# Optimization experiments

Measured on AMD Instinct MI355X. Metric: run time of the kernel, lower is better.

## Reference

```python
import jax, jax.numpy as jnp
import numpy as np

OUT_F = 2048
IN_F = 2048
NNZ = 209715  # int(0.05 * OUT_F * IN_F)
ALPHA = 1.0


def setup_inputs() -> dict:
    key = jax.random.key(0)
    k1, k2, k3, k4, k5, k6 = jax.random.split(key, 6)
    x = jax.random.normal(k1, (4, 4096, IN_F), dtype=jnp.float32)
    # two int4 nibbles (offset-by-8 codes in [0,15]) packed per byte
    base_packed = jax.random.randint(k2, (OUT_F, IN_F // 2), 0, 256, dtype=jnp.int32)
    # per-row scale = row_max/7, strictly positive
    scales = jax.random.uniform(k3, (OUT_F,), dtype=jnp.float32, minval=1e-3, maxval=0.1)
    # sparse residual in COO form (values are small corrections)
    ortho_vals = jax.random.normal(k4, (NNZ,), dtype=jnp.float32) * 0.01
    ortho_rows = jax.random.randint(k5, (NNZ,), 0, OUT_F, dtype=jnp.int32)
    ortho_cols = jax.random.randint(k6, (NNZ,), 0, IN_F, dtype=jnp.int32)
    return {"x": x, "base_packed": base_packed, "scales": scales,
            "ortho_vals": ortho_vals, "ortho_rows": ortho_rows, "ortho_cols": ortho_cols}


def _dequant_base(base_packed, scales):
    # unpack: low nibble -> even input cols, high nibble -> odd input cols
    low = base_packed & 0xF          # [out, in/2]
    high = (base_packed >> 4) & 0xF  # [out, in/2]
    w_offset = jnp.stack([low, high], axis=-1).reshape(OUT_F, IN_F)
    return (w_offset.astype(jnp.float32) - 8.0) * scales[:, None]  # [out, in]


def reference(x, base_packed, scales, ortho_vals, ortho_rows, ortho_cols):
    w_base = _dequant_base(base_packed, scales)
    # scatter sparse residual into dense weight (same size as weight itself)
    w_ortho = jnp.zeros((OUT_F, IN_F), dtype=jnp.float32).at[ortho_rows, ortho_cols].add(ortho_vals)
    W = w_base + ALPHA * w_ortho  # [out, in]
    x_flat = x.reshape(-1, IN_F)  # [tokens, in]
    out = jnp.einsum('ti,oi->to', x_flat, W)
    return out.reshape(x.shape[:-1] + (OUT_F,))
```

## Files before the change

kernel.cpp:

```cpp
#include <hip/hip_runtime.h>
#include <hip/hip_bf16.h>

#define OUT_F 2048
#define IN_F  2048

typedef __attribute__((ext_vector_type(8))) short bfx8;
typedef __attribute__((ext_vector_type(4))) short s16x4;
typedef __attribute__((ext_vector_type(4))) float fx4;

__device__ __forceinline__ unsigned short f2bf(float f) {
  unsigned int u = __float_as_uint(f);
  u += 0x7FFFu + ((u >> 16) & 1u);
  return (unsigned short)(u >> 16);
}

__device__ __forceinline__ void async_copy16(const void* gsrc, void* ldst) {
  __builtin_amdgcn_global_load_lds(
      (const __attribute__((address_space(1))) unsigned int*)gsrc,
      (__attribute__((address_space(3))) unsigned int*)ldst,
      16, 0, 0);
}


__global__ __launch_bounds__(256) void k_dequant(const int* __restrict__ packed,
                                                 const float* __restrict__ scales,
                                                 float* __restrict__ Wf) {
  int i = blockIdx.x * 256 + threadIdx.x;
  int row = i >> 10;
  int v = packed[i];
  float s = scales[row];
  float2 w;
  w.x = (float)((v & 0xF) - 8) * s;
  w.y = (float)(((v >> 4) & 0xF) - 8) * s;
  reinterpret_cast<float2*>(Wf)[i] = w;
}

__global__ __launch_bounds__(256) void k_scatter(const float* __restrict__ vals,
                                                 const int* __restrict__ rows,
                                                 const int* __restrict__ cols,
                                                 float* __restrict__ Wf, int nnz) {
  int i = blockIdx.x * 256 + threadIdx.x;
  if (i < nnz)
    atomicAdd(Wf + (size_t)rows[i] * IN_F + cols[i], vals[i]);
}

__global__ __launch_bounds__(256) void k_f32_to_bf16x8(const float* __restrict__ in,
                                                       short* __restrict__ outp) {
  long long i = (long long)blockIdx.x * 256 + threadIdx.x;
  const float4* v = reinterpret_cast<const float4*>(in) + 2 * i;
  float4 a = v[0], b = v[1];
  bfx8 r;
  r[0] = (short)f2bf(a.x); r[1] = (short)f2bf(a.y);
  r[2] = (short)f2bf(a.z); r[3] = (short)f2bf(a.w);
  r[4] = (short)f2bf(b.x); r[5] = (short)f2bf(b.y);
  r[6] = (short)f2bf(b.z); r[7] = (short)f2bf(b.w);
  reinterpret_cast<bfx8*>(outp)[i] = r;
}


__global__ __launch_bounds__(256) void k_gemm_bt(const short* __restrict__ A,
                                                 const short* __restrict__ B,
                                                 float* __restrict__ C,
                                                 int M, int N, int K) {
  __shared__ __align__(16) short Asm[128 * 32];
  __shared__ __align__(16) short Bsm[128 * 32];

  const int tid  = threadIdx.x;
  const int lane = tid & 63;
  const int wave = tid >> 6;
  const int wr = wave >> 1, wc = wave & 1;
  const int l15 = lane & 15, l16 = lane >> 4;

  int nwg = gridDim.x, bid = blockIdx.x;
  int swz = ((nwg & 7) == 0) ? ((bid & 7) * (nwg >> 3) + (bid >> 3)) : bid;
  int nbn = N / 128;
  int bm = swz / nbn, bn = swz % nbn;

  fx4 acc[4][4] = {};

  const short* Ablk = A + (size_t)bm * 128 * K;
  const short* Bblk = B + (size_t)bn * 128 * K;

  for (int k0 = 0; k0 < K; k0 += 32) {
#pragma unroll
    for (int i = 0; i < 2; ++i) {
      int c = i * 256 + tid;
      int r = c >> 2, kc = (c & 3) * 8;
      const short* ga = Ablk + (size_t)r * K + k0 + kc;
      const short* gb = Bblk + (size_t)r * K + k0 + kc;
      short* la = Asm + i * 2048 + wave * 512;
      short* lb = Bsm + i * 2048 + wave * 512;
      async_copy16(ga, la);
      async_copy16(gb, lb);
    }
    __syncthreads();

    bfx8 a[4], b[4];
#pragma unroll
    for (int mi = 0; mi < 4; ++mi)
      a[mi] = *reinterpret_cast<const bfx8*>(Asm + (wr * 64 + mi * 16 + l15) * 32 + l16 * 8);
#pragma unroll
    for (int ni = 0; ni < 4; ++ni)
      b[ni] = *reinterpret_cast<const bfx8*>(Bsm + (wc * 64 + ni * 16 + l15) * 32 + l16 * 8);
#pragma unroll
    for (int mi = 0; mi < 4; ++mi)
#pragma unroll
      for (int ni = 0; ni < 4; ++ni)
        acc[mi][ni] = __builtin_amdgcn_mfma_f32_16x16x32_bf16(a[mi], b[ni], acc[mi][ni], 0, 0, 0);
    __syncthreads();
  }

  float* Cblk = C + (size_t)(bm * 128 + wr * 64) * N + bn * 128 + wc * 64;
#pragma unroll
  for (int mi = 0; mi < 4; ++mi)
#pragma unroll
    for (int ni = 0; ni < 4; ++ni)
#pragma unroll
      for (int r = 0; r < 4; ++r)
        Cblk[(size_t)(mi * 16 + l16 * 4 + r) * N + ni * 16 + l15] = acc[mi][ni][r];
}

__global__ __launch_bounds__(256) void k_gemm_bt_cvtA(const float* __restrict__ A,
                                                      const short* __restrict__ B,
                                                      float* __restrict__ C,
                                                      int M, int N, int K) {
  __shared__ __align__(16) short Asm[128 * 32];
  __shared__ __align__(16) short Bsm[128 * 32];

  const int tid  = threadIdx.x;
  const int lane = tid & 63;
  const int wave = tid >> 6;
  const int wr = wave >> 1, wc = wave & 1;
  const int l15 = lane & 15, l16 = lane >> 4;

  int nwg = gridDim.x, bid = blockIdx.x;
  int swz = ((nwg & 7) == 0) ? ((bid & 7) * (nwg >> 3) + (bid >> 3)) : bid;
  int nbn = N / 128;
  int bm = swz / nbn, bn = swz % nbn;

  fx4 acc[4][4] = {};

  const float* Ablk = A + (size_t)bm * 128 * K;
  const short* Bblk = B + (size_t)bn * 128 * K;

  for (int k0 = 0; k0 < K; k0 += 32) {
#pragma unroll
    for (int i = 0; i < 2; ++i) {
      int c = i * 256 + tid;
      int r = c >> 2, kc = (c & 3) * 8;
      const short* gb = Bblk + (size_t)r * K + k0 + kc;
      short* lb = Bsm + i * 2048 + wave * 512;
      async_copy16(gb, lb);
    }
#pragma unroll
    for (int i = 0; i < 4; ++i) {
      int c = i * 256 + tid;
      int r = c >> 3, kc = (c & 7) * 4;
      float4 v = *reinterpret_cast<const float4*>(Ablk + (size_t)r * K + k0 + kc);
      s16x4 p;
      p[0] = (short)f2bf(v.x); p[1] = (short)f2bf(v.y);
      p[2] = (short)f2bf(v.z); p[3] = (short)f2bf(v.w);
      *reinterpret_cast<s16x4*>(Asm + r * 32 + kc) = p;
    }
    __syncthreads();

    bfx8 a[4], b[4];
#pragma unroll
    for (int mi = 0; mi < 4; ++mi)
      a[mi] = *reinterpret_cast<const bfx8*>(Asm + (wr * 64 + mi * 16 + l15) * 32 + l16 * 8);
#pragma unroll
    for (int ni = 0; ni < 4; ++ni)
      b[ni] = *reinterpret_cast<const bfx8*>(Bsm + (wc * 64 + ni * 16 + l15) * 32 + l16 * 8);
#pragma unroll
    for (int mi = 0; mi < 4; ++mi)
#pragma unroll
      for (int ni = 0; ni < 4; ++ni)
        acc[mi][ni] = __builtin_amdgcn_mfma_f32_16x16x32_bf16(a[mi], b[ni], acc[mi][ni], 0, 0, 0);
    __syncthreads();
  }

  float* Cblk = C + (size_t)(bm * 128 + wr * 64) * N + bn * 128 + wc * 64;
#pragma unroll
  for (int mi = 0; mi < 4; ++mi)
#pragma unroll
    for (int ni = 0; ni < 4; ++ni)
#pragma unroll
      for (int r = 0; r < 4; ++r)
        Cblk[(size_t)(mi * 16 + l16 * 4 + r) * N + ni * 16 + l15] = acc[mi][ni][r];
}

extern "C" void kernel_launch(void* const* d_in, const int* in_sizes, int n_in,
                              void* d_out, int out_size, void* d_ws, size_t ws_size,
                              hipStream_t stream) {
  const float* x      = (const float*)d_in[0];
  const int*   packed = (const int*)d_in[1];
  const float* scales = (const float*)d_in[2];
  const float* ovals  = (const float*)d_in[3];
  const int*   orows  = (const int*)d_in[4];
  const int*   ocols  = (const int*)d_in[5];
  float* out = (float*)d_out;

  const int tokens = in_sizes[0] / IN_F;
  const int nnz    = in_sizes[3];

  const size_t xb_bytes = (size_t)tokens * IN_F * sizeof(short);
  const size_t wf_bytes = (size_t)OUT_F * IN_F * sizeof(float);
  const size_t wb_bytes = (size_t)OUT_F * IN_F * sizeof(short);

  char* ws = (char*)d_ws;
  const int grid = (tokens / 128) * (OUT_F / 128);

  if (ws_size >= xb_bytes + wf_bytes + wb_bytes) {
    short* xb = (short*)ws;
    float* Wf = (float*)(ws + xb_bytes);
    short* Wb = (short*)(ws + xb_bytes + wf_bytes);

    k_dequant<<<OUT_F * IN_F / 2 / 256, 256, 0, stream>>>(packed, scales, Wf);
    k_scatter<<<(nnz + 255) / 256, 256, 0, stream>>>(ovals, orows, ocols, Wf, nnz);
    k_f32_to_bf16x8<<<OUT_F * IN_F / 8 / 256, 256, 0, stream>>>(Wf, Wb);
    k_f32_to_bf16x8<<<(int)((size_t)tokens * IN_F / 8 / 256), 256, 0, stream>>>(x, xb);
    k_gemm_bt<<<grid, 256, 0, stream>>>(xb, Wb, out, tokens, OUT_F, IN_F);
  } else {
    float* Wf = (float*)ws;
    short* Wb = (short*)(ws + wf_bytes);

    k_dequant<<<OUT_F * IN_F / 2 / 256, 256, 0, stream>>>(packed, scales, Wf);
    k_scatter<<<(nnz + 255) / 256, 256, 0, stream>>>(ovals, orows, ocols, Wf, nnz);
    k_f32_to_bf16x8<<<OUT_F * IN_F / 8 / 256, 256, 0, stream>>>(Wf, Wb);
    k_gemm_bt_cvtA<<<grid, 256, 0, stream>>>(x, Wb, out, tokens, OUT_F, IN_F);
  }
}
```

Baseline: 448.7 us.

## Replace GEMM with 256x256-tile double-buffered swizzled-LDS bf16 MFMA kernel

Replaces the 128x128, K=32 GEMM with a 512-thread kernel that computes 256x256 output tiles using K=64 steps. LDS is double-buffered so the next tile's async global->LDS copies overlap the current tile's MFMAs, and an XOR swizzle on LDS rows avoids bank conflicts. It also raises wave priority around the MFMA block. The fallback path for small workspaces is dropped, so the kernel now assumes the workspace is large enough for the bf16 copy of x.

```diff
diff --git a/kernel.cpp b/kernel.cpp
--- a/kernel.cpp
+++ b/kernel.cpp
@@ -5,7 +5,6 @@
 #define IN_F  2048
 
 typedef __attribute__((ext_vector_type(8))) short bfx8;
-typedef __attribute__((ext_vector_type(4))) short s16x4;
 typedef __attribute__((ext_vector_type(4))) float fx4;
 
 __device__ __forceinline__ unsigned short f2bf(float f) {
@@ -58,135 +57,108 @@
 }
 
 
-__global__ __launch_bounds__(256) void k_gemm_bt(const short* __restrict__ A,
-                                                 const short* __restrict__ B,
-                                                 float* __restrict__ C,
-                                                 int M, int N, int K) {
-  __shared__ __align__(16) short Asm[128 * 32];
-  __shared__ __align__(16) short Bsm[128 * 32];
+__global__ __launch_bounds__(512, 2) void k_gemm256(const short* __restrict__ A,
+                                                    const short* __restrict__ B,
+                                                    float* __restrict__ C,
+                                                    int M, int N, int K) {
+  extern __shared__ short smem[];
+  short* As = smem;
+  short* Bs = smem + 2 * 256 * 64;
 
-  const int tid  = threadIdx.x;
-  const int lane = tid & 63;
-  const int wave = tid >> 6;
-  const int wr = wave >> 1, wc = wave & 1;
-  const int l15 = lane & 15, l16 = lane >> 4;
+  const int tid = threadIdx.x;
+  const int l   = tid & 63;
+  const int w   = tid >> 6;
+  const int wr  = w >> 2;
+  const int wc  = w & 3;
+  const int l15 = l & 15, l16 = l >> 4;
 
   int nwg = gridDim.x, bid = blockIdx.x;
   int swz = ((nwg & 7) == 0) ? ((bid & 7) * (nwg >> 3) + (bid >> 3)) : bid;
-  int nbn = N / 128;
+  int nbn = N >> 8;
   int bm = swz / nbn, bn = swz % nbn;
 
-  fx4 acc[4][4] = {};
+  const short* Ablk = A + (size_t)bm * 256 * K;
+  const short* Bblk = B + (size_t)bn * 256 * K;
 
-  const short* Ablk = A + (size_t)bm * 128 * K;
-  const short* Bblk = B + (size_t)bn * 128 * K;
+  const int srow   = l >> 3;
+  const int srcoff = (((l & 7) ^ (l >> 3)) << 3);
 
-  for (int k0 = 0; k0 < K; k0 += 32) {
+  fx4 acc[8][4] = {};
+  const int NT = K >> 6;
+
 #pragma unroll
-    for (int i = 0; i < 2; ++i) {
-      int c = i * 256 + tid;
-      int r = c >> 2, kc = (c & 3) * 8;
-      const short* ga = Ablk + (size_t)r * K + k0 + kc;
-      const short* gb = Bblk + (size_t)r * K + k0 + kc;
-      short* la = Asm + i * 2048 + wave * 512;
-      short* lb = Bsm + i * 2048 + wave * 512;
-      async_copy16(ga, la);
-      async_copy16(gb, lb);
+  for (int h = 0; h < 2; ++h)
+#pragma unroll
+    for (int j = 0; j < 2; ++j) {
+      int row = h * 128 + w * 16 + j * 8;
+      async_copy16(Ablk + (size_t)(row + srow) * K + srcoff, As + row * 64);
+      async_copy16(Bblk + (size_t)(row + srow) * K + srcoff, Bs + row * 64);
     }
-    __syncthreads();
+  asm volatile("s_waitcnt vmcnt(0)" ::: "memory");
+  __builtin_amdgcn_s_barrier();
 
-    bfx8 a[4], b[4];
+  for (int kt = 0; kt < NT; ++kt) {
+    const int c = kt & 1;
+    const short* Ac = As + c * 256 * 64;
+    const short* Bc = Bs + c * 256 * 64;
+
+    __builtin_amdgcn_s_barrier();
+    __builtin_amdgcn_sched_barrier(0);
+
+    if (kt + 1 < NT) {
+      const int k0 = (kt + 1) << 6;
+      short* An = As + (c ^ 1) * 256 * 64;
+      short* Bn = Bs + (c ^ 1) * 256 * 64;
 #pragma unroll
-    for (int mi = 0; mi < 4; ++mi)
-      a[mi] = *reinterpret_cast<const bfx8*>(Asm + (wr * 64 + mi * 16 + l15) * 32 + l16 * 8);
+      for (int h = 0; h < 2; ++h)
 #pragma unroll
-    for (int ni = 0; ni < 4; ++ni)
-      b[ni] = *reinterpret_cast<const bfx8*>(Bsm + (wc * 64 + ni * 16 + l15) * 32 + l16 * 8);
+        for (int j = 0; j < 2; ++j) {
+          int row = h * 128 + w * 16 + j * 8;
+          async_copy16(Ablk + (size_t)(row + srow) * K + k0 + srcoff, An + row * 64);
+          async_copy16(Bblk + (size_t)(row + srow) * K + k0 + srcoff, Bn + row * 64);
+        }
+      asm volatile("s_waitcnt vmcnt(8)" ::: "memory");
+    } else {
+      asm volatile("s_waitcnt vmcnt(0)" ::: "memory");
+    }
+    __builtin_amdgcn_s_barrier();
+    __builtin_amdgcn_sched_barrier(0);
+
+    bfx8 bf[2][4];
 #pragma unroll
-    for (int mi = 0; mi < 4; ++mi)
+    for (int ks = 0; ks < 2; ++ks)
+#pragma unroll
+      for (int ni = 0; ni < 4; ++ni) {
+        int r = wc * 64 + ni * 16 + l15;
+        bf[ks][ni] = *reinterpret_cast<const bfx8*>(
+            Bc + r * 64 + (((ks * 4 + l16) ^ (l15 & 7)) << 3));
+      }
+    __builtin_amdgcn_s_setprio(1);
+#pragma unroll
+    for (int mi = 0; mi < 8; ++mi) {
+      int r = wr * 128 + mi * 16 + l15;
+      bfx8 a0 = *reinterpret_cast<const bfx8*>(
+          Ac + r * 64 + ((l16 ^ (l15 & 7)) << 3));
+      bfx8 a1 = *reinterpret_cast<const bfx8*>(
+          Ac + r * 64 + (((4 + l16) ^ (l15 & 7)) << 3));
 #pragma unroll
       for (int ni = 0; ni < 4; ++ni)
-        acc[mi][ni] = __builtin_amdgcn_mfma_f32_16x16x32_bf16(a[mi], b[ni], acc[mi][ni], 0, 0, 0);
-    __syncthreads();
+        acc[mi][ni] = __builtin_amdgcn_mfma_f32_16x16x32_bf16(a0, bf[0][ni], acc[mi][ni], 0, 0, 0);
+#pragma unroll
+      for (int ni = 0; ni < 4; ++ni)
+        acc[mi][ni] = __builtin_amdgcn_mfma_f32_16x16x32_bf16(a1, bf[1][ni], acc[mi][ni], 0, 0, 0);
+    }
+    __builtin_amdgcn_s_setprio(0);
   }
 
-  float* Cblk = C + (size_t)(bm * 128 + wr * 64) * N + bn * 128 + wc * 64;
+  float* Cb = C + (size_t)(bm * 256 + wr * 128) * N + bn * 256 + wc * 64;
 #pragma unroll
-  for (int mi = 0; mi < 4; ++mi)
+  for (int mi = 0; mi < 8; ++mi)
 #pragma unroll
     for (int ni = 0; ni < 4; ++ni)
 #pragma unroll
       for (int r = 0; r < 4; ++r)
-        Cblk[(size_t)(mi * 16 + l16 * 4 + r) * N + ni * 16 + l15] = acc[mi][ni][r];
-}
-
-__global__ __launch_bounds__(256) void k_gemm_bt_cvtA(const float* __restrict__ A,
-                                                      const short* __restrict__ B,
-                                                      float* __restrict__ C,
-                                                      int M, int N, int K) {
-  __shared__ __align__(16) short Asm[128 * 32];
-  __shared__ __align__(16) short Bsm[128 * 32];
-
-  const int tid  = threadIdx.x;
-  const int lane = tid & 63;
-  const int wave = tid >> 6;
-  const int wr = wave >> 1, wc = wave & 1;
-  const int l15 = lane & 15, l16 = lane >> 4;
-
-  int nwg = gridDim.x, bid = blockIdx.x;
-  int swz = ((nwg & 7) == 0) ? ((bid & 7) * (nwg >> 3) + (bid >> 3)) : bid;
-  int nbn = N / 128;
-  int bm = swz / nbn, bn = swz % nbn;
-
-  fx4 acc[4][4] = {};
-
-  const float* Ablk = A + (size_t)bm * 128 * K;
-  const short* Bblk = B + (size_t)bn * 128 * K;
-
-  for (int k0 = 0; k0 < K; k0 += 32) {
-#pragma unroll
-    for (int i = 0; i < 2; ++i) {
-      int c = i * 256 + tid;
-      int r = c >> 2, kc = (c & 3) * 8;
-      const short* gb = Bblk + (size_t)r * K + k0 + kc;
-      short* lb = Bsm + i * 2048 + wave * 512;
-      async_copy16(gb, lb);
-    }
-#pragma unroll
-    for (int i = 0; i < 4; ++i) {
-      int c = i * 256 + tid;
-      int r = c >> 3, kc = (c & 7) * 4;
-      float4 v = *reinterpret_cast<const float4*>(Ablk + (size_t)r * K + k0 + kc);
-      s16x4 p;
-      p[0] = (short)f2bf(v.x); p[1] = (short)f2bf(v.y);
-      p[2] = (short)f2bf(v.z); p[3] = (short)f2bf(v.w);
-      *reinterpret_cast<s16x4*>(Asm + r * 32 + kc) = p;
-    }
-    __syncthreads();
-
-    bfx8 a[4], b[4];
-#pragma unroll
-    for (int mi = 0; mi < 4; ++mi)
-      a[mi] = *reinterpret_cast<const bfx8*>(Asm + (wr * 64 + mi * 16 + l15) * 32 + l16 * 8);
-#pragma unroll
-    for (int ni = 0; ni < 4; ++ni)
-      b[ni] = *reinterpret_cast<const bfx8*>(Bsm + (wc * 64 + ni * 16 + l15) * 32 + l16 * 8);
-#pragma unroll
-    for (int mi = 0; mi < 4; ++mi)
-#pragma unroll
-      for (int ni = 0; ni < 4; ++ni)
-        acc[mi][ni] = __builtin_amdgcn_mfma_f32_16x16x32_bf16(a[mi], b[ni], acc[mi][ni], 0, 0, 0);
-    __syncthreads();
-  }
-
-  float* Cblk = C + (size_t)(bm * 128 + wr * 64) * N + bn * 128 + wc * 64;
-#pragma unroll
-  for (int mi = 0; mi < 4; ++mi)
-#pragma unroll
-    for (int ni = 0; ni < 4; ++ni)
-#pragma unroll
-      for (int r = 0; r < 4; ++r)
-        Cblk[(size_t)(mi * 16 + l16 * 4 + r) * N + ni * 16 + l15] = acc[mi][ni][r];
+        Cb[(size_t)(mi * 16 + l16 * 4 + r) * N + ni * 16 + l15] = acc[mi][ni][r];
 }
 
 extern "C" void kernel_launch(void* const* d_in, const int* in_sizes, int n_in,
@@ -205,28 +177,22 @@
 
   const size_t xb_bytes = (size_t)tokens * IN_F * sizeof(short);
   const size_t wf_bytes = (size_t)OUT_F * IN_F * sizeof(float);
-  const size_t wb_bytes = (size_t)OUT_F * IN_F * sizeof(short);
 
   char* ws = (char*)d_ws;
-  const int grid = (tokens / 128) * (OUT_F / 128);
+  short* xb = (short*)ws;
+  float* Wf = (float*)(ws + xb_bytes);
+  short* Wb = (short*)(ws + xb_bytes + wf_bytes);
 
-  if (ws_size >= xb_bytes + wf_bytes + wb_bytes) {
-    short* xb = (short*)ws;
-    float* Wf = (float*)(ws + xb_bytes);
-    short* Wb = (short*)(ws + xb_bytes + wf_bytes);
+  static_assert(sizeof(short) == 2, "");
+  const int lds_bytes = 2 * 2 * 256 * 64 * (int)sizeof(short);
+  (void)hipFuncSetAttribute((const void*)k_gemm256,
+                            hipFuncAttributeMaxDynamicSharedMemorySize, lds_bytes);
 
-    k_dequant<<<OUT_F * IN_F / 2 / 256, 256, 0, stream>>>(packed, scales, Wf);
-    k_scatter<<<(nnz + 255) / 256, 256, 0, stream>>>(ovals, orows, ocols, Wf, nnz);
-    k_f32_to_bf16x8<<<OUT_F * IN_F / 8 / 256, 256, 0, stream>>>(Wf, Wb);
-    k_f32_to_bf16x8<<<(int)((size_t)tokens * IN_F / 8 / 256), 256, 0, stream>>>(x, xb);
-    k_gemm_bt<<<grid, 256, 0, stream>>>(xb, Wb, out, tokens, OUT_F, IN_F);
-  } else {
-    float* Wf = (float*)ws;
-    short* Wb = (short*)(ws + wf_bytes);
+  k_dequant<<<OUT_F * IN_F / 2 / 256, 256, 0, stream>>>(packed, scales, Wf);
+  k_scatter<<<(nnz + 255) / 256, 256, 0, stream>>>(ovals, orows, ocols, Wf, nnz);
+  k_f32_to_bf16x8<<<OUT_F * IN_F / 8 / 256, 256, 0, stream>>>(Wf, Wb);
+  k_f32_to_bf16x8<<<(int)((size_t)tokens * IN_F / 8 / 256), 256, 0, stream>>>(x, xb);
 
-    k_dequant<<<OUT_F * IN_F / 2 / 256, 256, 0, stream>>>(packed, scales, Wf);
-    k_scatter<<<(nnz + 255) / 256, 256, 0, stream>>>(ovals, orows, ocols, Wf, nnz);
-    k_f32_to_bf16x8<<<OUT_F * IN_F / 8 / 256, 256, 0, stream>>>(Wf, Wb);
-    k_gemm_bt_cvtA<<<grid, 256, 0, stream>>>(x, Wb, out, tokens, OUT_F, IN_F);
-  }
+  const int grid = (tokens / 256) * (OUT_F / 256);
+  k_gemm256<<<grid, 512, lds_bytes, stream>>>(xb, Wb, out, tokens, OUT_F, IN_F);
 }
```

Measured after the change: 384.2 us. -14.4%, faster.
